# Optimization experiments

Hardware: AMD Instinct MI355X
Metric: run time of the kernel (lower is better)

The kernel has to match this reference:

```python
import jax, jax.numpy as jnp
import numpy as np

VEC = 64
HEADS = 16
DUP = 4
HIDDEN = VEC * HEADS * DUP  # 4096
EPS = 1e-12


def setup_inputs() -> dict:
    key = jax.random.key(0)
    ks = jax.random.split(key, 7)
    B, S, N = 4, 512, 512
    out_len = VEC * HEADS
    return {
        "embeddings": jax.random.normal(ks[0], (B, S, HIDDEN), jnp.float32),
        "keys": jax.random.normal(ks[1], (B, N, out_len), jnp.float32),
        "values": jax.random.normal(ks[2], (B, N, out_len), jnp.float32),
        "Wq": jax.random.normal(ks[3], (HIDDEN, HIDDEN), jnp.float32) * (1.0 / np.sqrt(HIDDEN)),
        "bq": jnp.zeros((HIDDEN,), jnp.float32),
        "Wre": jax.random.normal(ks[4], (HIDDEN, HIDDEN), jnp.float32) * (1.0 / np.sqrt(HIDDEN)),
        "bre": jnp.zeros((HIDDEN,), jnp.float32),
        "ln_g": jnp.ones((HIDDEN,), jnp.float32),
        "ln_b": jnp.zeros((HIDDEN,), jnp.float32),
    }


def reference(embeddings, keys, values, Wq, bq, Wre, bre, ln_g, ln_b):
    B, S, _ = embeddings.shape
    N = keys.shape[1]
    # query projection: (B,S,hidden) -> reshape to (B, S*DUP, VEC, HEADS) -> (B,H,S*DUP,VEC)
    q = embeddings @ Wq.T + bq
    q = q.reshape(B, S * DUP, VEC, HEADS).transpose(0, 3, 1, 2)
    # keys: (B,N,VEC*HEADS) -> (B,H,VEC,N); values -> (B,H,N,VEC)
    k = keys.reshape(B, N, VEC, HEADS).transpose(0, 3, 2, 1)
    v = values.reshape(B, N, VEC, HEADS).transpose(0, 3, 1, 2)
    scores = jnp.matmul(q, k) / np.sqrt(VEC).astype(np.float32)  # (B,H,S*DUP,N)
    probs = jax.nn.softmax(scores, axis=-1)
    out = jnp.matmul(probs, v)  # (B,H,S*DUP,VEC)
    # (B,H,S*DUP,VEC) -> (B,H,S,VEC*DUP) -> (B,S,H,VEC*DUP) -> (B,S,HIDDEN)
    out = out.reshape(B, HEADS, S, VEC * DUP).transpose(0, 2, 1, 3).reshape(B, S, HIDDEN)
    # LayerNorm (biased variance, torch semantics)
    mu = jnp.mean(out, axis=-1, keepdims=True)
    var = jnp.mean(jnp.square(out - mu), axis=-1, keepdims=True)
    ln = (out - mu) / jnp.sqrt(var + EPS) * ln_g + ln_b
    return ln @ Wre.T + bre
```

## Files before the change

kernel.cpp:

```cpp
#include <hip/hip_runtime.h>

typedef unsigned short u16;
typedef unsigned int   u32;
typedef __attribute__((ext_vector_type(8))) _Float16 half8;
typedef __attribute__((ext_vector_type(4))) _Float16 half4;
typedef __attribute__((ext_vector_type(4))) float    floatx4;

#define GLD16(g, l)                                                            \
  __builtin_amdgcn_global_load_lds(                                            \
      (const __attribute__((address_space(1))) void*)(g),                      \
      (__attribute__((address_space(3))) void*)(l), 16, 0, 0)

__global__ __launch_bounds__(256) void cvt_f16(const float* __restrict__ in,
                                               _Float16* __restrict__ out,
                                               int n8) {
  int i = blockIdx.x * 256 + threadIdx.x;
  if (i >= n8) return;
  const float4* p = (const float4*)in + (size_t)i * 2;
  float4 a = p[0], b = p[1];
  half8 h;
  h[0] = (_Float16)a.x; h[1] = (_Float16)a.y; h[2] = (_Float16)a.z; h[3] = (_Float16)a.w;
  h[4] = (_Float16)b.x; h[5] = (_Float16)b.y; h[6] = (_Float16)b.z; h[7] = (_Float16)b.w;
  *(half8*)(out + (size_t)i * 8) = h;
}

__global__ __launch_bounds__(256) void prep_kv(const float* __restrict__ keys,
                                               const float* __restrict__ values,
                                               _Float16* __restrict__ Kh,
                                               _Float16* __restrict__ Vt) {
  int tid = blockIdx.x * 256 + threadIdx.x;
  {
    int v = tid & 63, n = (tid >> 6) & 511, h = (tid >> 15) & 15, b = tid >> 19;
    Kh[tid] = (_Float16)keys[((size_t)(b * 512 + n)) * 1024 + v * 16 + h];
  }
  {
    int n = tid & 511, v = (tid >> 9) & 63, h = (tid >> 15) & 15, b = tid >> 19;
    Vt[tid] = (_Float16)values[((size_t)(b * 512 + n)) * 1024 + v * 16 + h];
  }
}

template <int MODE>
__global__ __launch_bounds__(256) void gemm_bt(const _Float16* __restrict__ A,
                                               const _Float16* __restrict__ Bw,
                                               float* __restrict__ Cf,
                                               _Float16* __restrict__ H0,
                                               _Float16* __restrict__ H1) {
  const int N = 4096, K = 4096;
  __shared__ _Float16 lA[128 * 32];
  __shared__ _Float16 lB[128 * 32];
  const int t = threadIdx.x;
  const int lane = t & 63;
  const int w = t >> 6;
  const int m0 = blockIdx.y * 128, n0 = blockIdx.x * 128;
  const int kb = blockIdx.z * 2048;
  const int wm = (w >> 1) * 64, wn = (w & 1) * 64;
  const int fr = lane & 15, fq = lane >> 4;

  floatx4 acc[4][4];
#pragma unroll
  for (int i = 0; i < 4; i++)
#pragma unroll
    for (int j = 0; j < 4; j++) acc[i][j] = (floatx4)(0.f);

  const int r0 = t >> 2;
  const int kc0 = (((t & 3) - ((t >> 3) & 3)) & 3) * 8;
  const _Float16* gA = A + (size_t)(m0 + r0) * K + kb + kc0;
  const _Float16* gB = Bw + (size_t)(n0 + r0) * K + kb + kc0;
  _Float16* dA = &lA[t * 8];
  _Float16* dB = &lB[t * 8];
  const int kof = ((fq + ((fr >> 1) & 3)) & 3) * 8;

  for (int k0 = 0; k0 < 2048; k0 += 32) {
    GLD16(gA, dA);
    GLD16(gA + (size_t)64 * K, dA + 2048);
    GLD16(gB, dB);
    GLD16(gB + (size_t)64 * K, dB + 2048);
    gA += 32;
    gB += 32;
    __syncthreads();
    half8 af[4], bf[4];
#pragma unroll
    for (int i = 0; i < 4; i++)
      af[i] = *(const half8*)&lA[(wm + i * 16 + fr) * 32 + kof];
#pragma unroll
    for (int j = 0; j < 4; j++)
      bf[j] = *(const half8*)&lB[(wn + j * 16 + fr) * 32 + kof];
#pragma unroll
    for (int i = 0; i < 4; i++)
#pragma unroll
      for (int j = 0; j < 4; j++)
        acc[i][j] =
            __builtin_amdgcn_mfma_f32_16x16x32_f16(af[i], bf[j], acc[i][j], 0, 0, 0);
    __syncthreads();
  }

  const int z = blockIdx.z;
#pragma unroll
  for (int i = 0; i < 4; i++) {
#pragma unroll
    for (int j = 0; j < 4; j++) {
      const int col = n0 + wn + j * 16 + fr;
      const int rbase = m0 + wm + i * 16 + fq * 4;
      if (MODE == 0) {
        if (z == 0) {
#pragma unroll
          for (int r = 0; r < 4; r++)
            Cf[(size_t)(rbase + r) * N + col] = acc[i][j][r];
        } else {
#pragma unroll
          for (int r = 0; r < 4; r++)
            H1[(size_t)(rbase + r) * N + col] = (_Float16)acc[i][j][r];
        }
      } else {
        _Float16* dst = z ? H1 : H0;
        const int d = col >> 10, v = (col >> 4) & 63, h = col & 15;
#pragma unroll
        for (int r = 0; r < 4; r++) {
          const int row = rbase + r;
          const int b = row >> 9, s = row & 511;
          dst[(((size_t)(b * 16 + h) * 2048) + (s * 4 + d)) * 64 + v] =
              (_Float16)acc[i][j][r];
        }
      }
    }
  }
}

__global__ __launch_bounds__(256) void combine1(const _Float16* __restrict__ p0,
                                                const _Float16* __restrict__ p1,
                                                const float* __restrict__ bq,
                                                _Float16* __restrict__ q) {
  const int j8 = (blockIdx.x * 256 + threadIdx.x) * 8;
  half8 a = *(const half8*)(p0 + j8);
  half8 b = *(const half8*)(p1 + j8);
  const int v0 = j8 & 63;
  const int d = (j8 >> 6) & 3;
  const int h = (j8 >> 17) & 15;
  const int colbase = d * 1024 + v0 * 16 + h;
  half8 o;
#pragma unroll
  for (int r = 0; r < 8; r++)
    o[r] = (_Float16)(((float)a[r] + (float)b[r] + bq[colbase + r * 16]) * 0.125f);
  *(half8*)(q + j8) = o;
}

__global__ __launch_bounds__(256) void combine2(float* __restrict__ out,
                                                const _Float16* __restrict__ p1,
                                                const float* __restrict__ bre) {
  const int i4 = (blockIdx.x * 256 + threadIdx.x) * 4;
  float4 o = *(float4*)&out[i4];
  half4 p = *(const half4*)(p1 + i4);
  float4 bb = *(const float4*)&bre[i4 & 4095];
  o.x += (float)p[0] + bb.x;
  o.y += (float)p[1] + bb.y;
  o.z += (float)p[2] + bb.z;
  o.w += (float)p[3] + bb.w;
  *(float4*)&out[i4] = o;
}

__global__ __launch_bounds__(256) void attn_mfma(const _Float16* __restrict__ Q,
                                                 const _Float16* __restrict__ Kh,
                                                 const _Float16* __restrict__ Vt,
                                                 float* __restrict__ Out) {
  __shared__ _Float16 Pbuf[4][32][136];
  const int t = threadIdx.x, lane = t & 63, w = t >> 6;
  const int fr = lane & 15, fq = lane >> 4;
  const int bh = blockIdx.y, qt = blockIdx.x;
  const int b = bh >> 4, h = bh & 15;

  const _Float16* Qb = Q + ((size_t)bh * 2048 + qt * 128 + w * 32) * 64;
  const _Float16* Kb = Kh + (size_t)bh * 512 * 64;
  const _Float16* Vb = Vt + (size_t)bh * 64 * 512;

  half8 qf[2][2];
#pragma unroll
  for (int i = 0; i < 2; i++)
#pragma unroll
    for (int ks = 0; ks < 2; ks++)
      qf[i][ks] = *(const half8*)(Qb + (i * 16 + fr) * 64 + ks * 32 + fq * 8);

  floatx4 oacc[2][4];
  float l_acc[2][4];
#pragma unroll
  for (int i = 0; i < 2; i++)
#pragma unroll
    for (int j = 0; j < 4; j++) {
      oacc[i][j] = (floatx4)(0.f);
      l_acc[i][j] = 0.f;
    }

  for (int c0 = 0; c0 < 512; c0 += 128) {
    floatx4 sc[2][8];
#pragma unroll
    for (int i = 0; i < 2; i++)
#pragma unroll
      for (int j = 0; j < 8; j++) sc[i][j] = (floatx4)(0.f);
#pragma unroll
    for (int j = 0; j < 8; j++) {
      const _Float16* kr = Kb + (size_t)(c0 + j * 16 + fr) * 64 + fq * 8;
      half8 k0 = *(const half8*)kr;
      half8 k1 = *(const half8*)(kr + 32);
#pragma unroll
      for (int i = 0; i < 2; i++) {
        sc[i][j] = __builtin_amdgcn_mfma_f32_16x16x32_f16(qf[i][0], k0, sc[i][j], 0, 0, 0);
        sc[i][j] = __builtin_amdgcn_mfma_f32_16x16x32_f16(qf[i][1], k1, sc[i][j], 0, 0, 0);
      }
    }
#pragma unroll
    for (int i = 0; i < 2; i++)
#pragma unroll
      for (int j = 0; j < 8; j++)
#pragma unroll
        for (int r = 0; r < 4; r++) {
          float p = __expf(sc[i][j][r]);
          l_acc[i][r] += p;
          Pbuf[w][i * 16 + fq * 4 + r][j * 16 + fr] = (_Float16)p;
        }
#pragma unroll
    for (int kn = 0; kn < 4; kn++) {
      half8 pa[2];
#pragma unroll
      for (int i = 0; i < 2; i++)
        pa[i] = *(const half8*)&Pbuf[w][i * 16 + fr][kn * 32 + fq * 8];
#pragma unroll
      for (int jv = 0; jv < 4; jv++) {
        half8 vb = *(const half8*)(Vb + (size_t)(jv * 16 + fr) * 512 + c0 + kn * 32 + fq * 8);
#pragma unroll
        for (int i = 0; i < 2; i++)
          oacc[i][jv] = __builtin_amdgcn_mfma_f32_16x16x32_f16(pa[i], vb, oacc[i][jv], 0, 0, 0);
      }
    }
  }

#pragma unroll
  for (int i = 0; i < 2; i++)
#pragma unroll
    for (int r = 0; r < 4; r++) {
#pragma unroll
      for (int m = 8; m; m >>= 1)
        l_acc[i][r] += __shfl_xor(l_acc[i][r], m, 16);
    }
#pragma unroll
  for (int i = 0; i < 2; i++) {
#pragma unroll
    for (int r = 0; r < 4; r++) {
      const float inv = 1.f / l_acc[i][r];
      const int m2 = qt * 128 + w * 32 + i * 16 + fq * 4 + r;
      float* orow = Out + ((size_t)(b * 512 + (m2 >> 2))) * 4096 + h * 256 + (m2 & 3) * 64 + fr;
#pragma unroll
      for (int jv = 0; jv < 4; jv++) orow[jv * 16] = oacc[i][jv][r] * inv;
    }
  }
}

__global__ __launch_bounds__(256) void ln_kernel(const float* __restrict__ X,
                                                 const float* __restrict__ g,
                                                 const float* __restrict__ bb,
                                                 _Float16* __restrict__ Y) {
  const int row = blockIdx.x;
  const int t = threadIdx.x;
  const float* x = X + (size_t)row * 4096;
  float4 vals[4];
  float sum = 0.f, sq = 0.f;
#pragma unroll
  for (int c = 0; c < 4; c++) {
    vals[c] = *(const float4*)&x[c * 1024 + t * 4];
    sum += vals[c].x + vals[c].y + vals[c].z + vals[c].w;
    sq += vals[c].x * vals[c].x + vals[c].y * vals[c].y + vals[c].z * vals[c].z +
          vals[c].w * vals[c].w;
  }
#pragma unroll
  for (int off = 32; off > 0; off >>= 1) {
    sum += __shfl_down(sum, off, 64);
    sq += __shfl_down(sq, off, 64);
  }
  __shared__ float red[8];
  const int w = t >> 6;
  if ((t & 63) == 0) {
    red[w] = sum;
    red[4 + w] = sq;
  }
  __syncthreads();
  sum = red[0] + red[1] + red[2] + red[3];
  sq = red[4] + red[5] + red[6] + red[7];
  const float mu = sum * (1.f / 4096.f);
  float var = sq * (1.f / 4096.f) - mu * mu;
  var = fmaxf(var, 0.f);
  const float rstd = rsqrtf(var + 1e-12f);
#pragma unroll
  for (int c = 0; c < 4; c++) {
    const int j = c * 1024 + t * 4;
    float4 gg = *(const float4*)&g[j];
    float4 bv = *(const float4*)&bb[j];
    half4 y;
    y[0] = (_Float16)((vals[c].x - mu) * rstd * gg.x + bv.x);
    y[1] = (_Float16)((vals[c].y - mu) * rstd * gg.y + bv.y);
    y[2] = (_Float16)((vals[c].z - mu) * rstd * gg.z + bv.z);
    y[3] = (_Float16)((vals[c].w - mu) * rstd * gg.w + bv.w);
    *(half4*)&Y[(size_t)row * 4096 + j] = y;
  }
}

extern "C" void kernel_launch(void* const* d_in, const int* in_sizes, int n_in,
                              void* d_out, int out_size, void* d_ws,
                              size_t ws_size, hipStream_t stream) {
  const float* emb = (const float*)d_in[0];
  const float* keys = (const float*)d_in[1];
  const float* values = (const float*)d_in[2];
  const float* Wq = (const float*)d_in[3];
  const float* bq = (const float*)d_in[4];
  const float* Wre = (const float*)d_in[5];
  const float* bre = (const float*)d_in[6];
  const float* ln_g = (const float*)d_in[7];
  const float* ln_b = (const float*)d_in[8];
  float* out = (float*)d_out;

  char* ws = (char*)d_ws;
  _Float16* embH = (_Float16*)(ws);
  _Float16* WqH = (_Float16*)(ws + ((size_t)16 << 20));
  _Float16* p1q = (_Float16*)(ws + ((size_t)48 << 20));
  _Float16* p0q = (_Float16*)d_out;
  _Float16* qattn = (_Float16*)(ws);
  _Float16* Kh = (_Float16*)(ws + ((size_t)48 << 20));
  _Float16* Vt = (_Float16*)(ws + ((size_t)52 << 20));
  _Float16* lnH = (_Float16*)(ws + ((size_t)16 << 20));
  _Float16* WreH = (_Float16*)(ws + ((size_t)32 << 20));
  _Float16* p1o = (_Float16*)(ws);

  cvt_f16<<<4096, 256, 0, stream>>>(emb, embH, 8388608 / 8);
  cvt_f16<<<8192, 256, 0, stream>>>(Wq, WqH, 16777216 / 8);
  gemm_bt<1><<<dim3(32, 16, 2), 256, 0, stream>>>(embH, WqH, nullptr, p0q, p1q);
  combine1<<<4096, 256, 0, stream>>>(p0q, p1q, bq, qattn);
  prep_kv<<<8192, 256, 0, stream>>>(keys, values, Kh, Vt);
  attn_mfma<<<dim3(16, 64), 256, 0, stream>>>(qattn, Kh, Vt, out);
  ln_kernel<<<2048, 256, 0, stream>>>(out, ln_g, ln_b, lnH);
  cvt_f16<<<8192, 256, 0, stream>>>(Wre, WreH, 16777216 / 8);
  gemm_bt<0><<<dim3(32, 16, 2), 256, 0, stream>>>(lnH, WreH, out, nullptr, p1o);
  combine2<<<8192, 256, 0, stream>>>(out, p1o, bre);
}
```

Measured before the change: 533.2 us.

## Double GEMM K-tile to 64 with XOR swizzle; move Q scatter into combine1

```diff
diff --git a/kernel.cpp b/kernel.cpp
--- a/kernel.cpp
+++ b/kernel.cpp
@@ -1,7 +1,5 @@
 #include <hip/hip_runtime.h>
 
-typedef unsigned short u16;
-typedef unsigned int   u32;
 typedef __attribute__((ext_vector_type(8))) _Float16 half8;
 typedef __attribute__((ext_vector_type(4))) _Float16 half4;
 typedef __attribute__((ext_vector_type(4))) float    floatx4;
@@ -40,17 +38,15 @@
 }
 
 template <int MODE>
-__global__ __launch_bounds__(256) void gemm_bt(const _Float16* __restrict__ A,
-                                               const _Float16* __restrict__ Bw,
-                                               float* __restrict__ Cf,
-                                               _Float16* __restrict__ H0,
-                                               _Float16* __restrict__ H1) {
-  const int N = 4096, K = 4096;
-  __shared__ _Float16 lA[128 * 32];
-  __shared__ _Float16 lB[128 * 32];
-  const int t = threadIdx.x;
-  const int lane = t & 63;
-  const int w = t >> 6;
+__global__ __launch_bounds__(256, 3) void gemm_bt(const _Float16* __restrict__ A,
+                                                  const _Float16* __restrict__ Bw,
+                                                  float* __restrict__ Cf,
+                                                  _Float16* __restrict__ H0,
+                                                  _Float16* __restrict__ H1) {
+  const int K = 4096;
+  __shared__ _Float16 lA[128 * 64];
+  __shared__ _Float16 lB[128 * 64];
+  const int t = threadIdx.x, lane = t & 63, w = t >> 6;
   const int m0 = blockIdx.y * 128, n0 = blockIdx.x * 128;
   const int kb = blockIdx.z * 2048;
   const int wm = (w >> 1) * 64, wn = (w & 1) * 64;
@@ -62,86 +58,99 @@
 #pragma unroll
     for (int j = 0; j < 4; j++) acc[i][j] = (floatx4)(0.f);
 
-  const int r0 = t >> 2;
-  const int kc0 = (((t & 3) - ((t >> 3) & 3)) & 3) * 8;
-  const _Float16* gA = A + (size_t)(m0 + r0) * K + kb + kc0;
-  const _Float16* gB = Bw + (size_t)(n0 + r0) * K + kb + kc0;
+  const int srow = t >> 3;
+  const int sch = (t & 7) ^ (srow & 7);
+  const _Float16* gA = A + (size_t)(m0 + srow) * K + kb + sch * 8;
+  const _Float16* gB = Bw + (size_t)(n0 + srow) * K + kb + sch * 8;
   _Float16* dA = &lA[t * 8];
   _Float16* dB = &lB[t * 8];
-  const int kof = ((fq + ((fr >> 1) & 3)) & 3) * 8;
-
-  for (int k0 = 0; k0 < 2048; k0 += 32) {
+
+  for (int k0 = 0; k0 < 2048; k0 += 64) {
     GLD16(gA, dA);
-    GLD16(gA + (size_t)64 * K, dA + 2048);
+    GLD16(gA + (size_t)32 * K, dA + 2048);
+    GLD16(gA + (size_t)64 * K, dA + 4096);
+    GLD16(gA + (size_t)96 * K, dA + 6144);
     GLD16(gB, dB);
-    GLD16(gB + (size_t)64 * K, dB + 2048);
-    gA += 32;
-    gB += 32;
+    GLD16(gB + (size_t)32 * K, dB + 2048);
+    GLD16(gB + (size_t)64 * K, dB + 4096);
+    GLD16(gB + (size_t)96 * K, dB + 6144);
+    gA += 64;
+    gB += 64;
     __syncthreads();
-    half8 af[4], bf[4];
-#pragma unroll
-    for (int i = 0; i < 4; i++)
-      af[i] = *(const half8*)&lA[(wm + i * 16 + fr) * 32 + kof];
-#pragma unroll
-    for (int j = 0; j < 4; j++)
-      bf[j] = *(const half8*)&lB[(wn + j * 16 + fr) * 32 + kof];
-#pragma unroll
-    for (int i = 0; i < 4; i++)
-#pragma unroll
-      for (int j = 0; j < 4; j++)
-        acc[i][j] =
-            __builtin_amdgcn_mfma_f32_16x16x32_f16(af[i], bf[j], acc[i][j], 0, 0, 0);
+#pragma unroll
+    for (int ks = 0; ks < 2; ks++) {
+      half8 af[4], bf[4];
+#pragma unroll
+      for (int i = 0; i < 4; i++) {
+        const int rr = wm + i * 16 + fr;
+        af[i] = *(const half8*)&lA[rr * 64 + (((ks * 4 + fq) ^ (rr & 7)) * 8)];
+      }
+#pragma unroll
+      for (int j = 0; j < 4; j++) {
+        const int rr = wn + j * 16 + fr;
+        bf[j] = *(const half8*)&lB[rr * 64 + (((ks * 4 + fq) ^ (rr & 7)) * 8)];
+      }
+#pragma unroll
+      for (int i = 0; i < 4; i++)
+#pragma unroll
+        for (int j = 0; j < 4; j++)
+          acc[i][j] =
+              __builtin_amdgcn_mfma_f32_16x16x32_f16(af[i], bf[j], acc[i][j], 0, 0, 0);
+    }
     __syncthreads();
   }
 
   const int z = blockIdx.z;
 #pragma unroll
-  for (int i = 0; i < 4; i++) {
+  for (int i = 0; i < 4; i++)
 #pragma unroll
     for (int j = 0; j < 4; j++) {
       const int col = n0 + wn + j * 16 + fr;
       const int rbase = m0 + wm + i * 16 + fq * 4;
-      if (MODE == 0) {
-        if (z == 0) {
-#pragma unroll
-          for (int r = 0; r < 4; r++)
-            Cf[(size_t)(rbase + r) * N + col] = acc[i][j][r];
-        } else {
-#pragma unroll
-          for (int r = 0; r < 4; r++)
-            H1[(size_t)(rbase + r) * N + col] = (_Float16)acc[i][j][r];
-        }
+      if (MODE == 0 && z == 0) {
+#pragma unroll
+        for (int r = 0; r < 4; r++)
+          Cf[(size_t)(rbase + r) * 4096 + col] = acc[i][j][r];
       } else {
-        _Float16* dst = z ? H1 : H0;
-        const int d = col >> 10, v = (col >> 4) & 63, h = col & 15;
-#pragma unroll
-        for (int r = 0; r < 4; r++) {
-          const int row = rbase + r;
-          const int b = row >> 9, s = row & 511;
-          dst[(((size_t)(b * 16 + h) * 2048) + (s * 4 + d)) * 64 + v] =
-              (_Float16)acc[i][j][r];
-        }
-      }
-    }
-  }
+        _Float16* P = z ? H1 : H0;
+#pragma unroll
+        for (int r = 0; r < 4; r++)
+          P[(size_t)(rbase + r) * 4096 + col] = (_Float16)acc[i][j][r];
+      }
+    }
 }
 
 __global__ __launch_bounds__(256) void combine1(const _Float16* __restrict__ p0,
                                                 const _Float16* __restrict__ p1,
                                                 const float* __restrict__ bq,
                                                 _Float16* __restrict__ q) {
-  const int j8 = (blockIdx.x * 256 + threadIdx.x) * 8;
-  half8 a = *(const half8*)(p0 + j8);
-  half8 b = *(const half8*)(p1 + j8);
-  const int v0 = j8 & 63;
-  const int d = (j8 >> 6) & 3;
-  const int h = (j8 >> 17) & 15;
-  const int colbase = d * 1024 + v0 * 16 + h;
-  half8 o;
-#pragma unroll
-  for (int r = 0; r < 8; r++)
-    o[r] = (_Float16)(((float)a[r] + (float)b[r] + bq[colbase + r * 16]) * 0.125f);
-  *(half8*)(q + j8) = o;
+  __shared__ _Float16 T[4][16][80];
+  const int t = threadIdx.x, L = t & 63, w = t >> 6;
+  const int m = blockIdx.x, d = w;
+  const int b = m >> 9, s = m & 511;
+  const size_t src = (size_t)m * 4096 + d * 1024 + L * 16;
+  half8 a0 = *(const half8*)(p0 + src);
+  half8 a1 = *(const half8*)(p0 + src + 8);
+  half8 b0 = *(const half8*)(p1 + src);
+  half8 b1 = *(const half8*)(p1 + src + 8);
+  const float4* bqv = (const float4*)(bq + d * 1024 + L * 16);
+  float bias[16];
+#pragma unroll
+  for (int c = 0; c < 4; c++) {
+    float4 f = bqv[c];
+    bias[c * 4 + 0] = f.x; bias[c * 4 + 1] = f.y;
+    bias[c * 4 + 2] = f.z; bias[c * 4 + 3] = f.w;
+  }
+#pragma unroll
+  for (int h = 0; h < 8; h++) {
+    T[w][h][L] = (_Float16)(((float)a0[h] + (float)b0[h] + bias[h]) * 0.125f);
+    T[w][h + 8][L] =
+        (_Float16)(((float)a1[h] + (float)b1[h] + bias[h + 8]) * 0.125f);
+  }
+  const int h2 = L >> 2, c2 = L & 3;
+  _Float16* dst = q + (((size_t)(b * 16 + h2) * 2048) + s * 4 + d) * 64 + c2 * 8;
+  *(half8*)dst = *(const half8*)&T[w][h2][c2 * 8];
+  *(half8*)(dst + 32) = *(const half8*)&T[w][h2][32 + c2 * 8];
 }
 
 __global__ __launch_bounds__(256) void combine2(float* __restrict__ out,
@@ -318,23 +327,23 @@
   char* ws = (char*)d_ws;
   _Float16* embH = (_Float16*)(ws);
   _Float16* WqH = (_Float16*)(ws + ((size_t)16 << 20));
-  _Float16* p1q = (_Float16*)(ws + ((size_t)48 << 20));
-  _Float16* p0q = (_Float16*)d_out;
+  _Float16* P1q = (_Float16*)(ws + ((size_t)48 << 20));
+  _Float16* P0q = (_Float16*)d_out;
   _Float16* qattn = (_Float16*)(ws);
   _Float16* Kh = (_Float16*)(ws + ((size_t)48 << 20));
   _Float16* Vt = (_Float16*)(ws + ((size_t)52 << 20));
   _Float16* lnH = (_Float16*)(ws + ((size_t)16 << 20));
   _Float16* WreH = (_Float16*)(ws + ((size_t)32 << 20));
-  _Float16* p1o = (_Float16*)(ws);
+  _Float16* P1o = (_Float16*)(ws);
 
   cvt_f16<<<4096, 256, 0, stream>>>(emb, embH, 8388608 / 8);
   cvt_f16<<<8192, 256, 0, stream>>>(Wq, WqH, 16777216 / 8);
-  gemm_bt<1><<<dim3(32, 16, 2), 256, 0, stream>>>(embH, WqH, nullptr, p0q, p1q);
-  combine1<<<4096, 256, 0, stream>>>(p0q, p1q, bq, qattn);
+  gemm_bt<1><<<dim3(32, 16, 2), 256, 0, stream>>>(embH, WqH, nullptr, P0q, P1q);
+  combine1<<<2048, 256, 0, stream>>>(P0q, P1q, bq, qattn);
   prep_kv<<<8192, 256, 0, stream>>>(keys, values, Kh, Vt);
   attn_mfma<<<dim3(16, 64), 256, 0, stream>>>(qattn, Kh, Vt, out);
   ln_kernel<<<2048, 256, 0, stream>>>(out, ln_g, ln_b, lnH);
   cvt_f16<<<8192, 256, 0, stream>>>(Wre, WreH, 16777216 / 8);
-  gemm_bt<0><<<dim3(32, 16, 2), 256, 0, stream>>>(lnH, WreH, out, nullptr, p1o);
-  combine2<<<8192, 256, 0, stream>>>(out, p1o, bre);
-}
+  gemm_bt<0><<<dim3(32, 16, 2), 256, 0, stream>>>(lnH, WreH, out, nullptr, P1o);
+  combine2<<<8192, 256, 0, stream>>>(out, P1o, bre);
+}
```

New measurement: 485.7 us. 8.9% less time.
